# Kernel optimization log

Measured on AMD Instinct MI355X. Metric: run time of the kernel, lower is better.

Reference implementation:

```python
import jax, jax.numpy as jnp
import numpy as np

B, H, W = 8, 256, 256
NF = 64          # num_feat
E = 12           # num_expert
D = NF * 4       # token dim = 256
CD = D * E       # expanded dim = 3072


def _lrelu(x):
    return jnp.where(x >= 0, x, 0.2 * x)


def _conv(x, w, stride, pad):
    return jax.lax.conv_general_dilated(
        x, w, (stride, stride), [(pad, pad), (pad, pad)],
        dimension_numbers=('NCHW', 'OIHW', 'NCHW'))


def _bn(x, g, b):
    # training-mode BatchNorm2d: batch statistics over (N, H, W)
    m = jnp.mean(x, axis=(0, 2, 3), keepdims=True)
    v = jnp.var(x, axis=(0, 2, 3), keepdims=True)
    xn = (x - m) * jax.lax.rsqrt(v + 1e-5)
    return xn * g[None, :, None, None] + b[None, :, None, None]


def setup_inputs() -> dict:
    key = jax.random.key(0)
    ks = jax.random.split(key, 16)
    s = 0.05
    d = {}
    d['x'] = jax.random.normal(ks[0], (B, 3, H, W), jnp.float32)
    d['conv0_w'] = jax.random.normal(ks[1], (NF, 3, 3, 3)) * s
    d['conv0_b'] = jnp.zeros((NF,))
    d['conv1_w'] = jax.random.normal(ks[2], (NF, NF, 4, 4)) * s
    d['bn1_g'] = jnp.ones((NF,)); d['bn1_b'] = jnp.zeros((NF,))
    d['conv2_w'] = jax.random.normal(ks[3], (2 * NF, NF, 3, 3)) * s
    d['bn2_g'] = jnp.ones((2 * NF,)); d['bn2_b'] = jnp.zeros((2 * NF,))
    d['conv3_w'] = jax.random.normal(ks[4], (2 * NF, 2 * NF, 4, 4)) * s
    d['bn3_g'] = jnp.ones((2 * NF,)); d['bn3_b'] = jnp.zeros((2 * NF,))
    d['conv4_w'] = jax.random.normal(ks[5], (4 * NF, 2 * NF, 3, 3)) * s
    d['bn4_g'] = jnp.ones((4 * NF,)); d['bn4_b'] = jnp.zeros((4 * NF,))
    d['conv5_w'] = jax.random.normal(ks[6], (4 * NF, 4 * NF, 3, 3)) * s
    d['bn5_g'] = jnp.ones((4 * NF,)); d['bn5_b'] = jnp.zeros((4 * NF,))
    d['conv6_w'] = jax.random.normal(ks[7], (4 * NF, 4 * NF, 3, 3)) * s
    d['bn6_g'] = jnp.ones((4 * NF,)); d['bn6_b'] = jnp.zeros((4 * NF,))
    d['w_gating'] = jax.random.normal(ks[8], (D, E))          # torch.randn init
    d['body_w'] = jax.random.normal(ks[9], (D, CD)) * s       # Linear(c_dim, c_dim*blocks)
    d['body_b'] = jnp.zeros((CD,))
    d['ortho_w'] = jax.random.normal(ks[10], (1, 1, CD))      # OrthorTransform weight
    d['cls_w1'] = jax.random.normal(ks[11], (D, NF // 2)) * s # shared classifier
    d['cls_b1'] = jnp.zeros((NF // 2,))
    d['cls_w2'] = jax.random.normal(ks[12], (NF // 2, 1)) * s
    d['cls_b2'] = jnp.zeros((1,))
    return d


def reference(x, conv0_w, conv0_b, conv1_w, bn1_g, bn1_b, conv2_w, bn2_g, bn2_b,
              conv3_w, bn3_g, bn3_b, conv4_w, bn4_g, bn4_b, conv5_w, bn5_g, bn5_b,
              conv6_w, bn6_g, bn6_b, w_gating, body_w, body_b, ortho_w,
              cls_w1, cls_b1, cls_w2, cls_b2):
    # --- FE conv stack ---
    h = _lrelu(_conv(x, conv0_w, 1, 1) + conv0_b[None, :, None, None])
    h = _lrelu(_bn(_conv(h, conv1_w, 2, 1), bn1_g, bn1_b))
    h = _lrelu(_bn(_conv(h, conv2_w, 1, 1), bn2_g, bn2_b))
    h = _lrelu(_bn(_conv(h, conv3_w, 2, 1), bn3_g, bn3_b))
    h = _lrelu(_bn(_conv(h, conv4_w, 1, 1), bn4_g, bn4_b))
    h = _lrelu(_bn(_conv(h, conv5_w, 1, 1), bn5_g, bn5_b))
    h = _lrelu(_bn(_conv(h, conv6_w, 1, 1), bn6_g, bn6_b))
    b, c, hh, ww = h.shape
    tok = h.reshape(b, c, hh * ww).transpose(0, 2, 1)            # (B, N, D)
    # --- softmax router ---
    routing = jax.nn.softmax(jnp.einsum('bnd,de->bne', tok, w_gating), axis=-1)
    # --- CodeReduction: Linear + lrelu, OrthorTransform multiply, lrelu ---
    feat = _lrelu(tok @ body_w + body_b)                         # (B, N, E*D)
    feat = _lrelu(feat * ortho_w)
    feat = feat.reshape(b, hh * ww, E, D)                        # torch.split chunks
    # --- shared expert MLP on every chunk (all classifiers alias one module) ---
    hid = _lrelu(jnp.einsum('bned,df->bnef', feat, cls_w1) + cls_b1)
    outs = (jnp.einsum('bnef,fo->bneo', hid, cls_w2) + cls_b2)[..., 0]  # (B,N,E)
    # --- top-1 select (equivalent to the torch.where cascade) ---
    idx = jnp.argmax(routing, axis=-1, keepdims=True)
    output = jnp.take_along_axis(outs, idx, axis=-1)             # (B, N, 1)
    return output
```

## Files before the change

### kernel.cpp

```cpp
#include <hip/hip_runtime.h>

__device__ __forceinline__ float lrelu(float x) { return x >= 0.f ? x : 0.2f * x; }

typedef const __attribute__((address_space(1))) void* gas_ptr;
typedef __attribute__((address_space(3))) void* las_ptr;

__global__ __launch_bounds__(256) void conv0_k(const float* __restrict__ x,
                                               const float* __restrict__ w,
                                               const float* __restrict__ bias,
                                               float* __restrict__ out) {
    __shared__ float sIn[3][34][34];
    __shared__ float sW[27][16];
    const int H = 256;
    int tid = threadIdx.x, tx = tid & 31, ty = tid >> 5;
    int tX = (blockIdx.x & 7) * 32, tY = (blockIdx.x >> 3) * 32;
    int b = blockIdx.y, cog = blockIdx.z * 16;
    float acc[4][16] = {};
    const float* inB = x + (size_t)b * 3 * H * H;
    for (int idx = tid; idx < 3 * 1156; idx += 256) {
        int ci = idx / 1156, r = idx % 1156, iy = r / 34, ix = r % 34;
        int gy = tY - 1 + iy, gx = tX - 1 + ix;
        float v = 0.f;
        if ((unsigned)gy < 256u && (unsigned)gx < 256u)
            v = inB[(ci * H + gy) * H + gx];
        sIn[ci][iy][ix] = v;
    }
    for (int idx = tid; idx < 27 * 16; idx += 256) {
        int co = idx & 15, rest = idx >> 4;
        sW[rest][co] = w[(cog + co) * 27 + rest];
    }
    __syncthreads();
#pragma unroll
    for (int ci = 0; ci < 3; ci++)
#pragma unroll
        for (int dy = 0; dy < 3; dy++)
#pragma unroll
            for (int dx = 0; dx < 3; dx++) {
                float a0 = sIn[ci][ty + dy][tx + dx];
                float a1 = sIn[ci][ty + 8 + dy][tx + dx];
                float a2 = sIn[ci][ty + 16 + dy][tx + dx];
                float a3 = sIn[ci][ty + 24 + dy][tx + dx];
                const float* wp = sW[ci * 9 + dy * 3 + dx];
#pragma unroll
                for (int co = 0; co < 16; co++) {
                    float wv = wp[co];
                    acc[0][co] += a0 * wv; acc[1][co] += a1 * wv;
                    acc[2][co] += a2 * wv; acc[3][co] += a3 * wv;
                }
            }
    float* outB = out + (size_t)(b * 64 + cog) * 67080;
#pragma unroll
    for (int co = 0; co < 16; co++) {
        float bv = bias[cog + co];
#pragma unroll
        for (int r = 0; r < 4; r++)
            outB[(size_t)co * 67080 + (size_t)(tY + ty + 8 * r + 1) * 260 +
                 tX + tx + 1] = lrelu(acc[r][co] + bv);
    }
}

template <int COG, int RPT, int NWV>
__device__ __forceinline__ void stats_epi(float (&acc)[RPT][COG], float2* sRed,
                                          double2* part, int cog, int slotBase,
                                          int S, int tid) {
    const int lane = tid & 63, wv = tid >> 6;
    float s[COG], q[COG];
#pragma unroll
    for (int c = 0; c < COG; c++) {
        float ss = 0.f, qq = 0.f;
#pragma unroll
        for (int j = 0; j < RPT; j++) { float v = acc[j][c]; ss += v; qq += v * v; }
        s[c] = ss; q[c] = qq;
    }
#pragma unroll
    for (int off = 32; off; off >>= 1)
#pragma unroll
        for (int c = 0; c < COG; c++) {
            s[c] += __shfl_xor(s[c], off);
            q[c] += __shfl_xor(q[c], off);
        }
    if (lane == 0)
#pragma unroll
        for (int c = 0; c < COG; c++) sRed[wv * COG + c] = make_float2(s[c], q[c]);
    __syncthreads();
    if (tid < COG) {
        double ss = 0.0, qq = 0.0;
#pragma unroll
        for (int wvi = 0; wvi < NWV; wvi++) {
            float2 p = sRed[wvi * COG + tid];
            ss += (double)p.x; qq += (double)p.y;
        }
        int slot = slotBase + blockIdx.y * gridDim.x + blockIdx.x;
        part[(size_t)(cog + tid) * S + slot] = make_double2(ss, qq);
    }
}

template <int COG>
__global__ __launch_bounds__(256) void c4x4p_k(const float* __restrict__ in,
                                               const float* __restrict__ w,
                                               float* __restrict__ out,
                                               double2* __restrict__ part,
                                               int slotBase, int S,
                                               int Cin, int Cout, int Hin,
                                               int Hp, int Wp,
                                               int oHp, int oWp, int oOff) {
    __shared__ float sIn[2][4488];
    __shared__ float sW[2][16 * COG];
    __shared__ float2 sRed[4 * COG];
    const int Hout = Hin >> 1;
    const int tid = threadIdx.x, tx = tid & 31, ty = tid >> 5;
    const int tpr = Hout >> 5;
    const int tX = (blockIdx.x % tpr) * 32, tY = (blockIdx.x / tpr) * 32;
    const int b = blockIdx.y, cog = blockIdx.z * COG;
    const int HWin = Hp * Wp;
    const float* inB = in + (size_t)b * Cin * HWin;
    const int wvbase = tid & ~63;

    int gOff[5]; int lOff[5]; bool act[5];
#pragma unroll
    for (int r = 0; r < 5; r++) {
        int idx = tid + r * 256;
        bool a = idx < 1122;
        int row = idx / 17, c4 = idx % 17;
        gOff[r] = a ? ((2 * tY + row) * Wp + 2 * tX + 4 * c4) : 0;
        lOff[r] = (r * 256 + wvbase) * 4;
        act[r] = a;
    }
    const int wco = tid % COG, wt = tid / COG;
    const int wgo = ((cog + wco) * Cin) * 16 + wt;
    const bool wact = tid < 16 * COG;

    float acc[4][COG];
#pragma unroll
    for (int j = 0; j < 4; j++)
#pragma unroll
        for (int c = 0; c < COG; c++) acc[j][c] = 0.f;

#pragma unroll
    for (int r = 0; r < 5; r++)
        if (act[r])
            __builtin_amdgcn_global_load_lds((gas_ptr)(inB + gOff[r]),
                                             (las_ptr)(&sIn[0][lOff[r]]), 16, 0, 0);
    if (wact)
        __builtin_amdgcn_global_load_lds((gas_ptr)(w + wgo),
                                         (las_ptr)(&sW[0][wvbase]), 4, 0, 0);
    __syncthreads();

    for (int k = 0; k < Cin; k++) {
        const int cur = k & 1, nb = cur ^ 1;
        const bool more = (k + 1) < Cin;
        if (more) {
            const float* p = inB + (size_t)(k + 1) * HWin;
#pragma unroll
            for (int r = 0; r < 5; r++)
                if (act[r])
                    __builtin_amdgcn_global_load_lds(
                        (gas_ptr)(p + gOff[r]),
                        (las_ptr)(&sIn[nb][lOff[r]]), 16, 0, 0);
            if (wact)
                __builtin_amdgcn_global_load_lds(
                    (gas_ptr)(w + wgo + (k + 1) * 16),
                    (las_ptr)(&sW[nb][wvbase]), 4, 0, 0);
        }
        const float* sI = sIn[cur];
        const float* sw = sW[cur];
#pragma unroll
        for (int dy = 0; dy < 4; dy++)
#pragma unroll
            for (int dx = 0; dx < 4; dx++) {
                const float* bp = sI + (2 * ty + dy) * 68 + 2 * tx + dx;
                float a0 = bp[0];
                float a1 = bp[16 * 68];
                float a2 = bp[32 * 68];
                float a3 = bp[48 * 68];
                const float* wp = sw + (dy * 4 + dx) * COG;
#pragma unroll
                for (int c = 0; c < COG; c++) {
                    float wv = wp[c];
                    acc[0][c] += a0 * wv; acc[1][c] += a1 * wv;
                    acc[2][c] += a2 * wv; acc[3][c] += a3 * wv;
                }
            }
        __syncthreads();
    }

    float* outB = out + (size_t)(b * Cout + cog) * oHp * oWp;
#pragma unroll
    for (int c = 0; c < COG; c++)
#pragma unroll
        for (int r = 0; r < 4; r++)
            outB[(size_t)c * oHp * oWp +
                 (size_t)(tY + ty + 8 * r + oOff) * oWp + tX + tx + oOff] =
                acc[r][c];
    stats_epi<COG, 4, 4>(acc, sRed, part, cog, slotBase, S, tid);
}

template <int COG>
__global__ __launch_bounds__(256) void c3x3_k(const float* __restrict__ in,
                                              const float* __restrict__ w,
                                              float* __restrict__ out,
                                              double2* __restrict__ part,
                                              int slotBase, int S,
                                              int Cin, int Cout, int H,
                                              int Hp, int Wp,
                                              int oHp, int oWp, int oOff) {
    constexpr int RS = 36;
    constexpr int ROWS = 66;
    constexpr int CI = ROWS * RS;
    constexpr int NSF4 = 2 * ROWS * 9;
    constexpr int NR = 5;
    __shared__ float sIn[2][2 * CI];
    __shared__ float sW[2][18 * COG];
    __shared__ float2 sRed[4 * COG];
    const int tid = threadIdx.x, tx = tid & 31, ty = tid >> 5;
    const int tpr = H >> 5;
    const int tX = (blockIdx.x % tpr) * 32, tY = (blockIdx.x / tpr) * 64;
    const int b = blockIdx.y, cog = blockIdx.z * COG;
    const int HWin = Hp * Wp;
    const float* inB = in + (size_t)b * Cin * HWin;
    const int wvbase = tid & ~63;

    int gOff[NR]; int lOff[NR]; bool act[NR];
#pragma unroll
    for (int r = 0; r < NR; r++) {
        int idx = tid + r * 256;
        act[r] = idx < NSF4;
        int ci = idx / (9 * ROWS), rem = idx % (9 * ROWS);
        int row = rem / 9, c4 = rem % 9;
        gOff[r] = act[r] ? (ci * HWin + (tY + row) * Wp + tX + 4 * c4) : 0;
        lOff[r] = (r * 256 + wvbase) * 4;
    }
    const bool wact = tid < 18 * COG;
    int wgo;
    {
        int co = tid % COG, rest = tid / COG;
        int ci = rest / 9, t = rest % 9;
        wgo = ((cog + co) * Cin + ci) * 9 + t;
    }

    float acc[8][COG];
#pragma unroll
    for (int j = 0; j < 8; j++)
#pragma unroll
        for (int c = 0; c < COG; c++) acc[j][c] = 0.f;

    const int steps = Cin >> 1;

    auto STAGE = [&](int t, int buf) {
        const float* p = inB + (size_t)(2 * t) * HWin;
#pragma unroll
        for (int r = 0; r < NR; r++)
            if (act[r])
                __builtin_amdgcn_global_load_lds(
                    (gas_ptr)(p + gOff[r]),
                    (las_ptr)(&sIn[buf][lOff[r]]), 16, 0, 0);
        if (wact)
            __builtin_amdgcn_global_load_lds(
                (gas_ptr)(w + (size_t)(2 * t) * 9 + wgo),
                (las_ptr)(&sW[buf][wvbase]), 4, 0, 0);
    };

    STAGE(0, 0);
    __syncthreads();
    for (int k = 0; k < steps; k++) {
        const int cur = k & 1, nb = cur ^ 1;
        if (k + 1 < steps) STAGE(k + 1, nb);
        const float* sI = sIn[cur];
        const float* sw = sW[cur];
#pragma unroll
        for (int ci = 0; ci < 2; ci++)
#pragma unroll
            for (int dx = 0; dx < 3; dx++) {
                const float* bp = sI + ci * CI + (8 * ty) * RS + tx + dx;
                float a[10];
#pragma unroll
                for (int j = 0; j < 10; j++) a[j] = bp[j * RS];
#pragma unroll
                for (int dy = 0; dy < 3; dy++) {
                    const float* wp = sw + (ci * 9 + dy * 3 + dx) * COG;
#pragma unroll
                    for (int c = 0; c < COG; c++) {
                        float wv = wp[c];
#pragma unroll
                        for (int j = 0; j < 8; j++)
                            acc[j][c] += a[j + dy] * wv;
                    }
                }
            }
        __syncthreads();
    }

    float* outB = out + (size_t)(b * Cout + cog) * oHp * oWp;
#pragma unroll
    for (int c = 0; c < COG; c++)
#pragma unroll
        for (int j = 0; j < 8; j++)
            outB[(size_t)c * oHp * oWp +
                 (size_t)(tY + 8 * ty + j + oOff) * oWp + tX + tx + oOff] =
                acc[j][c];
    stats_epi<COG, 8, 4>(acc, sRed, part, cog, slotBase, S, tid);
}

template <int COG>
__global__ __launch_bounds__(128) void c3x3h_k(const float* __restrict__ in,
                                               const float* __restrict__ w,
                                               float* __restrict__ out,
                                               double2* __restrict__ part,
                                               int slotBase, int S,
                                               int Cin, int Cout, int H,
                                               int Hp, int Wp,
                                               int oHp, int oWp, int oOff) {
    constexpr int RS = 36;
    constexpr int ROWS = 34;
    constexpr int CI = ROWS * RS;
    constexpr int NSF4 = 2 * ROWS * 9;
    constexpr int NR = (NSF4 + 127) / 128;
    constexpr int NWR = (18 * COG + 127) / 128;
    __shared__ float sIn[2][2 * CI];
    __shared__ float sW[2][18 * COG];
    __shared__ float2 sRed[2 * COG];
    const int tid = threadIdx.x, tx = tid & 31, ty = tid >> 5;
    const int tpr = H >> 5;
    const int tX = (blockIdx.x % tpr) * 32, tY = (blockIdx.x / tpr) * 32;
    const int b = blockIdx.y, cog = blockIdx.z * COG;
    const int HWin = Hp * Wp;
    const float* inB = in + (size_t)b * Cin * HWin;
    const int wvbase = tid & ~63;

    int gOff[NR]; int lOff[NR]; bool act[NR];
#pragma unroll
    for (int r = 0; r < NR; r++) {
        int idx = tid + r * 128;
        bool a = idx < NSF4;
        int ci = idx / (9 * ROWS), rem = idx % (9 * ROWS);
        int row = rem / 9, c4 = rem % 9;
        gOff[r] = a ? (ci * HWin + (tY + row) * Wp + tX + 4 * c4) : 0;
        lOff[r] = (r * 128 + wvbase) * 4;
        act[r] = a;
    }
    int wgo[NWR]; bool wact[NWR]; int wlo[NWR];
#pragma unroll
    for (int r = 0; r < NWR; r++) {
        int widx = tid + r * 128;
        bool a = widx < 18 * COG;
        int co = widx % COG, rest = widx / COG;
        int ci = rest / 9, t = rest % 9;
        wgo[r] = a ? (((cog + co) * Cin + ci) * 9 + t) : 0;
        wlo[r] = r * 128 + wvbase;
        wact[r] = a;
    }

    float acc[8][COG];
#pragma unroll
    for (int j = 0; j < 8; j++)
#pragma unroll
        for (int c = 0; c < COG; c++) acc[j][c] = 0.f;

    const int steps = Cin >> 1;

    auto STAGE = [&](int t, int buf) {
        const float* p = inB + (size_t)(2 * t) * HWin;
#pragma unroll
        for (int r = 0; r < NR; r++)
            if (act[r])
                __builtin_amdgcn_global_load_lds(
                    (gas_ptr)(p + gOff[r]),
                    (las_ptr)(&sIn[buf][lOff[r]]), 16, 0, 0);
        const float* wp2 = w + (size_t)(2 * t) * 9;
#pragma unroll
        for (int r = 0; r < NWR; r++)
            if (wact[r])
                __builtin_amdgcn_global_load_lds(
                    (gas_ptr)(wp2 + wgo[r]),
                    (las_ptr)(&sW[buf][wlo[r]]), 4, 0, 0);
    };

    STAGE(0, 0);
    __syncthreads();
    for (int k = 0; k < steps; k++) {
        const int cur = k & 1, nb = cur ^ 1;
        if (k + 1 < steps) STAGE(k + 1, nb);
        const float* sI = sIn[cur];
        const float* sw = sW[cur];
#pragma unroll
        for (int ci = 0; ci < 2; ci++)
#pragma unroll
            for (int dx = 0; dx < 3; dx++) {
                const float* bp = sI + ci * CI + (8 * ty) * RS + tx + dx;
                float a[10];
#pragma unroll
                for (int j = 0; j < 10; j++) a[j] = bp[j * RS];
#pragma unroll
                for (int dy = 0; dy < 3; dy++) {
                    const float* wp = sw + (ci * 9 + dy * 3 + dx) * COG;
#pragma unroll
                    for (int c = 0; c < COG; c++) {
                        float wv = wp[c];
#pragma unroll
                        for (int j = 0; j < 8; j++)
                            acc[j][c] += a[j + dy] * wv;
                    }
                }
            }
        __syncthreads();
    }

    float* outB = out + (size_t)(b * Cout + cog) * oHp * oWp;
#pragma unroll
    for (int c = 0; c < COG; c++)
#pragma unroll
        for (int j = 0; j < 8; j++)
            outB[(size_t)c * oHp * oWp +
                 (size_t)(tY + 8 * ty + j + oOff) * oWp + tX + tx + oOff] =
                acc[j][c];
    stats_epi<COG, 8, 2>(acc, sRed, part, cog, slotBase, S, tid);
}

__global__ __launch_bounds__(256) void bnact_k(float* __restrict__ p,
                                               const double2* __restrict__ part,
                                               int S, double invN,
                                               const float* __restrict__ g,
                                               const float* __restrict__ bb,
                                               int C, int H, int W,
                                               int Hp, int Wp) {
    __shared__ double2 red[4];
    __shared__ float2 sSS;
    int pc = blockIdx.x;
    int c = pc & (C - 1);
    int tid = threadIdx.x;
    const bool xf = (part != nullptr);
    if (xf) {
        double sum = 0.0, sq = 0.0;
        for (int s = tid; s < S; s += 256) {
            double2 pp = part[(size_t)c * S + s];
            sum += pp.x; sq += pp.y;
        }
#pragma unroll
        for (int off = 32; off; off >>= 1) {
            sum += __shfl_xor(sum, off);
            sq += __shfl_xor(sq, off);
        }
        if ((tid & 63) == 0) red[tid >> 6] = make_double2(sum, sq);
        __syncthreads();
        if (tid == 0) {
            double s2 = 0.0, q2 = 0.0;
#pragma unroll
            for (int wv = 0; wv < 4; wv++) { s2 += red[wv].x; q2 += red[wv].y; }
            double m = s2 * invN;
            double v = q2 * invN - m * m;
            double sc = (double)g[c] / sqrt(v + 1e-5);
            sSS = make_float2((float)sc, (float)((double)bb[c] - m * sc));
        }
        __syncthreads();
    }
    const float2 t = xf ? sSS : make_float2(1.f, 0.f);
    float4* pl4 = reinterpret_cast<float4*>(p + (size_t)pc * Hp * Wp);
    const int wq = Wp >> 2;
    const int n4 = Hp * wq;
    const float4 z4 = make_float4(0.f, 0.f, 0.f, 0.f);
    for (int i = tid; i < n4; i += 256) {
        int y = i / wq, xq = i - y * wq;
        if (!xf || y < 1 || y > H) {
            pl4[i] = z4;
            continue;
        }
        float4 v = pl4[i];
        float r0 = v.x, r1 = v.y, r2 = v.z, r3 = v.w;
        int x0 = xq << 2;
        r0 = (x0 >= 1 && x0 <= W) ? lrelu(t.x * r0 + t.y) : 0.f;
        r1 = (x0 + 1 <= W)        ? lrelu(t.x * r1 + t.y) : 0.f;
        r2 = (x0 + 2 <= W)        ? lrelu(t.x * r2 + t.y) : 0.f;
        r3 = (x0 + 3 <= W)        ? lrelu(t.x * r3 + t.y) : 0.f;
        pl4[i] = make_float4(r0, r1, r2, r3);
    }
}

__global__ __launch_bounds__(256) void transp_k(const float* __restrict__ h6,
                                                const double2* __restrict__ part,
                                                double invN,
                                                const float* __restrict__ g,
                                                const float* __restrict__ bb,
                                                float* __restrict__ tok) {
    __shared__ float sT[32][33];
    __shared__ float2 sSS[32];
    int tid = threadIdx.x;
    int tx = tid & 31, ty = tid >> 5;
    int n0 = blockIdx.x * 32, d0 = blockIdx.y * 32, b = blockIdx.z;
    {
        int d = tid >> 3, s = tid & 7;
        int c = d0 + d;
        double sum = 0.0, sq = 0.0;
#pragma unroll
        for (int i = 0; i < 4; i++) {
            double2 pp = part[(size_t)c * 32 + s + 8 * i];
            sum += pp.x; sq += pp.y;
        }
        sum += __shfl_xor(sum, 4); sq += __shfl_xor(sq, 4);
        sum += __shfl_xor(sum, 2); sq += __shfl_xor(sq, 2);
        sum += __shfl_xor(sum, 1); sq += __shfl_xor(sq, 1);
        if (s == 0) {
            double m = sum * invN;
            double v = sq * invN - m * m;
            double sc = (double)g[c] / sqrt(v + 1e-5);
            sSS[d] = make_float2((float)sc, (float)((double)bb[c] - m * sc));
        }
    }
    __syncthreads();
    const float* hb = h6 + ((size_t)b * 256 + d0) * 4096 + n0;
#pragma unroll
    for (int r = 0; r < 4; r++) {
        int d = ty + 8 * r;
        float2 t = sSS[d];
        sT[d][tx] = lrelu(t.x * hb[d * 4096 + tx] + t.y);
    }
    __syncthreads();
    float* tb = tok + ((size_t)b * 4096 + n0) * 256 + d0;
#pragma unroll
    for (int r = 0; r < 4; r++) {
        int n = ty + 8 * r;
        tb[n * 256 + tx] = sT[tx][n];
    }
}

__global__ __launch_bounds__(256) void token_k(const float* __restrict__ tok,
                                               const float* __restrict__ wg,
                                               const float* __restrict__ bw,
                                               const float* __restrict__ bb,
                                               const float* __restrict__ ow,
                                               const float* __restrict__ w1,
                                               const float* __restrict__ b1,
                                               const float* __restrict__ w2,
                                               const float* __restrict__ b2,
                                               float* __restrict__ outp) {
    __shared__ float sf[4][256];
    const int tid = threadIdx.x, wave = tid >> 6, l = tid & 63;
    const int t = blockIdx.x * 4 + wave;
    const float4 tv = reinterpret_cast<const float4*>(tok + (size_t)t * 256)[l];
    sf[wave][4 * l + 0] = tv.x; sf[wave][4 * l + 1] = tv.y;
    sf[wave][4 * l + 2] = tv.z; sf[wave][4 * l + 3] = tv.w;

    float lg[12];
#pragma unroll
    for (int e = 0; e < 12; e++) lg[e] = 0.f;
    const float tj[4] = {tv.x, tv.y, tv.z, tv.w};
#pragma unroll
    for (int j = 0; j < 4; j++) {
        const float* wr = wg + (4 * l + j) * 12;
#pragma unroll
        for (int e = 0; e < 12; e++) lg[e] += tj[j] * wr[e];
    }
#pragma unroll
    for (int off = 32; off > 0; off >>= 1) {
#pragma unroll
        for (int e = 0; e < 12; e++) lg[e] += __shfl_xor(lg[e], off);
    }
    int idx = 0; float best = lg[0];
#pragma unroll
    for (int e = 1; e < 12; e++)
        if (lg[e] > best) { best = lg[e]; idx = e; }
    const int cb = idx * 256;

    float f0 = 0.f, f1 = 0.f, f2 = 0.f, f3 = 0.f;
    const float* bwp = bw + cb + 4 * l;
#pragma unroll 4
    for (int d = 0; d < 256; d++) {
        const float td = sf[wave][d];
        const float4 wv = *reinterpret_cast<const float4*>(bwp + (size_t)d * 3072);
        f0 += td * wv.x; f1 += td * wv.y;
        f2 += td * wv.z; f3 += td * wv.w;
    }
    float fj[4] = {f0, f1, f2, f3};
#pragma unroll
    for (int j = 0; j < 4; j++) {
        int jj = cb + 4 * l + j;
        float v = lrelu(fj[j] + bb[jj]);
        v = lrelu(v * ow[jj]);
        sf[wave][4 * l + j] = v;
    }

    float o = 0.f;
    if (l < 32) {
        float h = b1[l];
#pragma unroll 4
        for (int j = 0; j < 256; j++) h += sf[wave][j] * w1[j * 32 + l];
        h = lrelu(h);
        o = h * w2[l];
    }
    o += __shfl_xor(o, 16); o += __shfl_xor(o, 8); o += __shfl_xor(o, 4);
    o += __shfl_xor(o, 2);  o += __shfl_xor(o, 1);
    if (l == 0) outp[t] = o + b2[0];
}

extern "C" void kernel_launch(void* const* d_in, const int* in_sizes, int n_in,
                              void* d_out, int out_size, void* d_ws, size_t ws_size,
                              hipStream_t stream) {
    const float* x   = (const float*)d_in[0];
    const float* w0  = (const float*)d_in[1];
    const float* b0  = (const float*)d_in[2];
    const float* w1  = (const float*)d_in[3];
    const float* g1  = (const float*)d_in[4];
    const float* be1 = (const float*)d_in[5];
    const float* w2  = (const float*)d_in[6];
    const float* g2  = (const float*)d_in[7];
    const float* be2 = (const float*)d_in[8];
    const float* w3  = (const float*)d_in[9];
    const float* g3  = (const float*)d_in[10];
    const float* be3 = (const float*)d_in[11];
    const float* w4  = (const float*)d_in[12];
    const float* g4  = (const float*)d_in[13];
    const float* be4 = (const float*)d_in[14];
    const float* w5  = (const float*)d_in[15];
    const float* g5  = (const float*)d_in[16];
    const float* be5 = (const float*)d_in[17];
    const float* w6  = (const float*)d_in[18];
    const float* g6  = (const float*)d_in[19];
    const float* be6 = (const float*)d_in[20];
    const float* wg  = (const float*)d_in[21];
    const float* bw  = (const float*)d_in[22];
    const float* bbp = (const float*)d_in[23];
    const float* owp = (const float*)d_in[24];
    const float* cw1 = (const float*)d_in[25];
    const float* cb1 = (const float*)d_in[26];
    const float* cw2 = (const float*)d_in[27];
    const float* cb2 = (const float*)d_in[28];

    char* W = (char*)d_ws;
    double2* part = (double2*)(W + 16384);

    char* BIG = W + 278528;
    float* h0p = (float*)(BIG);
    float* h1p = (float*)(BIG + 70287360);
    float* h2p = (float*)(BIG);
    float* h3p = (float*)(BIG + 70287360);
    float* h4p = (float*)(BIG);
    float* h5p = (float*)(BIG + 36765696);
    float* h6  = (float*)(BIG);
    float* tok = (float*)(BIG + 36765696);

    bnact_k<<<256, 256, 0, stream>>>(h0p, nullptr, 0, 0.0, nullptr, nullptr,
                                     64, 256, 256, 258, 260);
    for (int half = 0; half < 2; half++) {
        conv0_k<<<dim3(64, 4, 4), 256, 0, stream>>>(
            x + (size_t)half * 4 * 3 * 65536, w0, b0, h0p);
        c4x4p_k<8><<<dim3(16, 4, 8), 256, 0, stream>>>(
            h0p, w1, h1p + (size_t)half * 4 * 64 * 17160, part, half * 64, 128,
            64, 64, 256, 258, 260, 130, 132, 1);
    }
    bnact_k<<<512, 256, 0, stream>>>(h1p, part, 128, 1.0 / 131072.0, g1, be1,
                                     64, 128, 128, 130, 132);
    c3x3_k<8><<<dim3(8, 8, 16), 256, 0, stream>>>(
        h1p, w2, h2p, part, 0, 64, 64, 128, 128, 130, 132, 130, 132, 1);
    bnact_k<<<1024, 256, 0, stream>>>(h2p, part, 64, 1.0 / 131072.0, g2, be2,
                                      128, 128, 128, 130, 132);
    c4x4p_k<8><<<dim3(4, 8, 16), 256, 0, stream>>>(
        h2p, w3, h3p, part, 0, 32, 128, 128, 128, 130, 132, 66, 68, 1);
    bnact_k<<<1024, 256, 0, stream>>>(h3p, part, 32, 1.0 / 32768.0, g3, be3,
                                      128, 64, 64, 66, 68);
    c3x3h_k<8><<<dim3(4, 8, 32), 128, 0, stream>>>(
        h3p, w4, h4p, part, 0, 32, 128, 256, 64, 66, 68, 66, 68, 1);
    bnact_k<<<2048, 256, 0, stream>>>(h4p, part, 32, 1.0 / 32768.0, g4, be4,
                                      256, 64, 64, 66, 68);
    c3x3h_k<8><<<dim3(4, 8, 32), 128, 0, stream>>>(
        h4p, w5, h5p, part, 0, 32, 256, 256, 64, 66, 68, 66, 68, 1);
    bnact_k<<<2048, 256, 0, stream>>>(h5p, part, 32, 1.0 / 32768.0, g5, be5,
                                      256, 64, 64, 66, 68);
    c3x3h_k<8><<<dim3(4, 8, 32), 128, 0, stream>>>(
        h5p, w6, h6, part, 0, 32, 256, 256, 64, 66, 68, 64, 64, 0);
    transp_k<<<dim3(128, 8, 8), 256, 0, stream>>>(h6, part, 1.0 / 32768.0,
                                                  g6, be6, tok);
    token_k<<<8192, 256, 0, stream>>>(tok, wg, bw, bbp, owp, cw1, cb1, cw2, cb2,
                                      (float*)d_out);
}
```

Before: 2.391 ms.

## Split input channels across two half-blocks in 64x64 3x3 convs with LDS reduction

The 3x3 conv kernel for the 64x64 layers moves from 128 to 256 threads per block. Each half of the block handles half of the input channels with its own double-buffered LDS staging, and the partial sums are then combined through LDS before the output store and the stats epilogue. The aim is to double the wavefronts working on each tile and raise latency hiding for these conv layers, which launch only 1024 blocks. The cost is twice the LDS per block, which can lower the number of resident blocks, plus an extra reduction pass through shared memory with a barrier.

```diff
diff --git a/kernel.cpp b/kernel.cpp
--- a/kernel.cpp
+++ b/kernel.cpp
@@ -302,7 +302,7 @@
 }
 
 template <int COG>
-__global__ __launch_bounds__(128) void c3x3h_k(const float* __restrict__ in,
+__global__ __launch_bounds__(256) void c3x3s_k(const float* __restrict__ in,
                                                const float* __restrict__ w,
                                                float* __restrict__ out,
                                                double2* __restrict__ part,
@@ -314,23 +314,26 @@
     constexpr int ROWS = 34;
     constexpr int CI = ROWS * RS;
     constexpr int NSF4 = 2 * ROWS * 9;
-    constexpr int NR = (NSF4 + 127) / 128;
-    constexpr int NWR = (18 * COG + 127) / 128;
-    __shared__ float sIn[2][2 * CI];
-    __shared__ float sW[2][18 * COG];
-    __shared__ float2 sRed[2 * COG];
-    const int tid = threadIdx.x, tx = tid & 31, ty = tid >> 5;
+    constexpr int NR = 5;
+    constexpr int NWR = 2;
+    __shared__ float sIn[2][2][2 * CI];
+    __shared__ float sW[2][2][18 * COG];
+    __shared__ float2 sRed[4 * COG];
+    const int tid = threadIdx.x;
+    const int half = tid >> 7, htid = tid & 127;
+    const int tx = htid & 31, ty = htid >> 5;
     const int tpr = H >> 5;
     const int tX = (blockIdx.x % tpr) * 32, tY = (blockIdx.x / tpr) * 32;
     const int b = blockIdx.y, cog = blockIdx.z * COG;
     const int HWin = Hp * Wp;
-    const float* inB = in + (size_t)b * Cin * HWin;
-    const int wvbase = tid & ~63;
+    const int HC = Cin >> 1;
+    const float* inB = in + ((size_t)b * Cin + (size_t)half * HC) * HWin;
+    const int wvbase = htid & ~63;
 
     int gOff[NR]; int lOff[NR]; bool act[NR];
 #pragma unroll
     for (int r = 0; r < NR; r++) {
-        int idx = tid + r * 128;
+        int idx = htid + r * 128;
         bool a = idx < NSF4;
         int ci = idx / (9 * ROWS), rem = idx % (9 * ROWS);
         int row = rem / 9, c4 = rem % 9;
@@ -341,11 +344,11 @@
     int wgo[NWR]; bool wact[NWR]; int wlo[NWR];
 #pragma unroll
     for (int r = 0; r < NWR; r++) {
-        int widx = tid + r * 128;
+        int widx = htid + r * 128;
         bool a = widx < 18 * COG;
         int co = widx % COG, rest = widx / COG;
         int ci = rest / 9, t = rest % 9;
-        wgo[r] = a ? (((cog + co) * Cin + ci) * 9 + t) : 0;
+        wgo[r] = a ? (((cog + co) * Cin + half * HC + ci) * 9 + t) : 0;
         wlo[r] = r * 128 + wvbase;
         wact[r] = a;
     }
@@ -356,7 +359,7 @@
 #pragma unroll
         for (int c = 0; c < COG; c++) acc[j][c] = 0.f;
 
-    const int steps = Cin >> 1;
+    const int steps = HC >> 1;
 
     auto STAGE = [&](int t, int buf) {
         const float* p = inB + (size_t)(2 * t) * HWin;
@@ -365,14 +368,14 @@
             if (act[r])
                 __builtin_amdgcn_global_load_lds(
                     (gas_ptr)(p + gOff[r]),
-                    (las_ptr)(&sIn[buf][lOff[r]]), 16, 0, 0);
+                    (las_ptr)(&sIn[half][buf][lOff[r]]), 16, 0, 0);
         const float* wp2 = w + (size_t)(2 * t) * 9;
 #pragma unroll
         for (int r = 0; r < NWR; r++)
             if (wact[r])
                 __builtin_amdgcn_global_load_lds(
                     (gas_ptr)(wp2 + wgo[r]),
-                    (las_ptr)(&sW[buf][wlo[r]]), 4, 0, 0);
+                    (las_ptr)(&sW[half][buf][wlo[r]]), 4, 0, 0);
     };
 
     STAGE(0, 0);
@@ -380,8 +383,8 @@
     for (int k = 0; k < steps; k++) {
         const int cur = k & 1, nb = cur ^ 1;
         if (k + 1 < steps) STAGE(k + 1, nb);
-        const float* sI = sIn[cur];
-        const float* sw = sW[cur];
+        const float* sI = sIn[half][cur];
+        const float* sw = sW[half][cur];
 #pragma unroll
         for (int ci = 0; ci < 2; ci++)
 #pragma unroll
@@ -405,15 +408,39 @@
         __syncthreads();
     }
 
-    float* outB = out + (size_t)(b * Cout + cog) * oHp * oWp;
-#pragma unroll
-    for (int c = 0; c < COG; c++)
+    float* scratch = &sIn[0][0][0];
+    if (half == 1) {
 #pragma unroll
         for (int j = 0; j < 8; j++)
-            outB[(size_t)c * oHp * oWp +
-                 (size_t)(tY + 8 * ty + j + oOff) * oWp + tX + tx + oOff] =
-                acc[j][c];
-    stats_epi<COG, 8, 2>(acc, sRed, part, cog, slotBase, S, tid);
+#pragma unroll
+            for (int c = 0; c < COG; c++)
+                scratch[htid * 65 + j * COG + c] = acc[j][c];
+    }
+    __syncthreads();
+    if (half == 0) {
+#pragma unroll
+        for (int j = 0; j < 8; j++)
+#pragma unroll
+            for (int c = 0; c < COG; c++)
+                acc[j][c] += scratch[htid * 65 + j * COG + c];
+    } else {
+#pragma unroll
+        for (int j = 0; j < 8; j++)
+#pragma unroll
+            for (int c = 0; c < COG; c++) acc[j][c] = 0.f;
+    }
+
+    if (half == 0) {
+        float* outB = out + (size_t)(b * Cout + cog) * oHp * oWp;
+#pragma unroll
+        for (int c = 0; c < COG; c++)
+#pragma unroll
+            for (int j = 0; j < 8; j++)
+                outB[(size_t)c * oHp * oWp +
+                     (size_t)(tY + 8 * ty + j + oOff) * oWp + tX + tx + oOff] =
+                    acc[j][c];
+    }
+    stats_epi<COG, 8, 4>(acc, sRed, part, cog, slotBase, S, tid);
 }
 
 __global__ __launch_bounds__(256) void bnact_k(float* __restrict__ p,
@@ -656,15 +683,15 @@
         h2p, w3, h3p, part, 0, 32, 128, 128, 128, 130, 132, 66, 68, 1);
     bnact_k<<<1024, 256, 0, stream>>>(h3p, part, 32, 1.0 / 32768.0, g3, be3,
                                       128, 64, 64, 66, 68);
-    c3x3h_k<8><<<dim3(4, 8, 32), 128, 0, stream>>>(
+    c3x3s_k<8><<<dim3(4, 8, 32), 256, 0, stream>>>(
         h3p, w4, h4p, part, 0, 32, 128, 256, 64, 66, 68, 66, 68, 1);
     bnact_k<<<2048, 256, 0, stream>>>(h4p, part, 32, 1.0 / 32768.0, g4, be4,
                                       256, 64, 64, 66, 68);
-    c3x3h_k<8><<<dim3(4, 8, 32), 128, 0, stream>>>(
+    c3x3s_k<8><<<dim3(4, 8, 32), 256, 0, stream>>>(
         h4p, w5, h5p, part, 0, 32, 256, 256, 64, 66, 68, 66, 68, 1);
     bnact_k<<<2048, 256, 0, stream>>>(h5p, part, 32, 1.0 / 32768.0, g5, be5,
                                       256, 64, 64, 66, 68);
-    c3x3h_k<8><<<dim3(4, 8, 32), 128, 0, stream>>>(
+    c3x3s_k<8><<<dim3(4, 8, 32), 256, 0, stream>>>(
         h5p, w6, h6, part, 0, 32, 256, 256, 64, 66, 68, 64, 64, 0);
     transp_k<<<dim3(128, 8, 8), 256, 0, stream>>>(h6, part, 1.0 / 32768.0,
                                                   g6, be6, tok);
```

New measurement: 2.532 ms. +5.9%, slower.
